# Kernel optimization log

Hardware: AMD Instinct MI355X
Metric: run time of the kernel (lower is better)

Reference implementation:

```python
import jax, jax.numpy as jnp
import numpy as np

FIELD_DIMS = (339, 5825, 64)
RANK = 128
NUM_CHANNELS = 256
BATCH = 131072
NUM_MODES = len(FIELD_DIMS)


def setup_inputs() -> dict:
    key = jax.random.key(0)
    ks = jax.random.split(key, 12)
    # per-mode in-range indices, shape (B, num_modes)
    cols = [jax.random.randint(ks[i], (BATCH,), 0, FIELD_DIMS[i]) for i in range(NUM_MODES)]
    indices = jnp.stack(cols, axis=1).astype(jnp.int64)
    # embedding tables (one per tensor mode)
    emb0 = jax.random.normal(ks[3], (FIELD_DIMS[0], RANK), jnp.float32) * 0.1
    emb1 = jax.random.normal(ks[4], (FIELD_DIMS[1], RANK), jnp.float32) * 0.1
    emb2 = jax.random.normal(ks[5], (FIELD_DIMS[2], RANK), jnp.float32) * 0.1
    # conv1: Conv2d(1, C, kernel=(rank,1)) -> weight (C, rank) after squeeze
    w1 = jax.random.normal(ks[6], (NUM_CHANNELS, RANK), jnp.float32) * (1.0 / np.sqrt(RANK))
    b1 = jnp.zeros((NUM_CHANNELS,), jnp.float32)
    # conv2: Conv2d(C, C, kernel=(1,num_modes)) -> weight (C_out, C_in, num_modes)
    w2 = jax.random.normal(ks[7], (NUM_CHANNELS, NUM_CHANNELS, NUM_MODES), jnp.float32) * (1.0 / np.sqrt(NUM_CHANNELS * NUM_MODES))
    b2 = jnp.zeros((NUM_CHANNELS,), jnp.float32)
    # aggregation MLP
    wfc1 = jax.random.normal(ks[8], (NUM_CHANNELS, NUM_CHANNELS), jnp.float32) * (1.0 / np.sqrt(NUM_CHANNELS))
    bfc1 = jnp.zeros((NUM_CHANNELS,), jnp.float32)
    wfc2 = jax.random.normal(ks[9], (1, NUM_CHANNELS), jnp.float32) * (1.0 / np.sqrt(NUM_CHANNELS))
    bfc2 = jnp.zeros((1,), jnp.float32)
    return {"indices": indices, "emb0": emb0, "emb1": emb1, "emb2": emb2,
            "w1": w1, "b1": b1, "w2": w2, "b2": b2,
            "wfc1": wfc1, "bfc1": bfc1, "wfc2": wfc2, "bfc2": bfc2}


def reference(indices, emb0, emb1, emb2, w1, b1, w2, b2, wfc1, bfc1, wfc2, bfc2):
    # EmbeddingModule: (B, rank, num_modes)
    x = jnp.stack([emb0[indices[:, 0]], emb1[indices[:, 1]], emb2[indices[:, 2]]], axis=2)
    # conv1 over rank dim (kernel (rank,1)): (B, C, num_modes)
    h = jax.nn.relu(jnp.einsum('brm,cr->bcm', x, w1) + b1[None, :, None])
    # conv2 over mode dim (kernel (1,num_modes)): (B, C)
    h = jax.nn.relu(jnp.einsum('bcm,dcm->bd', h, w2) + b2)
    # AggregationModule MLP
    h = jax.nn.relu(h @ wfc1.T + bfc1)
    out = jax.nn.relu(h @ wfc2.T + bfc2)  # (B, 1)
    return out.squeeze(-1)  # (B,)
```

## Files before the change

kernel.cpp:

```cpp
#include <hip/hip_runtime.h>

typedef __bf16 bf16;
typedef __bf16 bf16x4 __attribute__((ext_vector_type(4)));
typedef __bf16 bf16x8 __attribute__((ext_vector_type(8)));
typedef float  f32x4  __attribute__((ext_vector_type(4)));
typedef unsigned int uint32;

#define BT 64

#define N_EF0 (22*2048)
#define N_EF1 (365*2048)
#define N_EF2 (4*2048)
#define O_EF0 0
#define O_EF1 (O_EF0+N_EF0)
#define O_EF2 (O_EF1+N_EF1)
#define O_W1F (O_EF2+N_EF2)
#define O_W2F (O_W1F+32768)
#define O_F1  (O_W2F+196608)
#define O_F2  (O_F1+65536)
#define N_TOT (O_F2+256)

#define BYTES_BF16 ((size_t)N_TOT*2)
#define OFF_FLOAT  BYTES_BF16
#define OFF_FLAG   (OFF_FLOAT + 772*4)
#define OFF_IDX    (OFF_FLAG + 16)
#define N_IDX      (131072*3)
#define OFF_Q      (OFF_IDX + (size_t)N_IDX*4)

#define QB0 0
#define QB1 (339*256)
#define QB2 (QB1 + 5825*256)

static __device__ __forceinline__ f32x4 mfma16(bf16x8 a, bf16x8 b, f32x4 c) {
    return __builtin_amdgcn_mfma_f32_16x16x32_bf16(a, b, c, 0, 0, 0);
}

static __device__ __forceinline__ unsigned frag_off(unsigned ee, unsigned kk, unsigned nks) {
    return (((ee >> 4) * nks + (kk >> 5)) * 64u + ((kk >> 3) & 3u) * 16u + (ee & 15u)) * 8u
           + (kk & 7u);
}

__global__ __launch_bounds__(256)
void convert_all(const void* __restrict__ e0, const void* __restrict__ e1,
                 const void* __restrict__ e2, const void* __restrict__ w1r,
                 const void* __restrict__ b1r, const void* __restrict__ w2r,
                 const void* __restrict__ b2r, const void* __restrict__ f1r,
                 const void* __restrict__ fc1br, const void* __restrict__ f2r,
                 const void* __restrict__ fc2br, const void* __restrict__ idxr,
                 bf16* __restrict__ wsb, float* __restrict__ wsf,
                 int* __restrict__ flagp, int* __restrict__ idx32)
{
    __shared__ int sF;
    const int tid = threadIdx.x;
    const int bid = blockIdx.x;
    if (tid == 0) sF = 0;
    __syncthreads();

    if (bid < 256) {
        if (((const uint32*)idxr)[tid * 2 + 1] != 0) atomicOr(&sF, 1);
        __syncthreads();
        const bool i64 = (sF == 0);
        #pragma unroll
        for (int it = 0; it < 6; ++it) {
            int k = bid * 1536 + it * 256 + tid;
            if (k < N_IDX) {
                long long v = i64 ? ((const long long*)idxr)[k]
                                  : (long long)((const int*)idxr)[k];
                int m = k - (k / 3) * 3;
                long long dim = (m == 0 ? 339 : (m == 1 ? 5825 : 64));
                v = v < 0 ? 0 : (v >= dim ? dim - 1 : v);
                idx32[k] = (int)v;
            }
        }
        return;
    }

    if (tid < 64) {
        uint32 e = (((const uint32*)w1r)[tid] >> 7) & 0xffu;
        if (e > 126u) atomicOr(&sF, 1);
    }
    __syncthreads();
    const bool fp32 = (sF != 0);

    if (bid < 768) {
        const unsigned n4 = 895744u / 4u;
        for (unsigned u = (bid - 256) * 256u + tid; u < n4; u += 512u * 256u) {
            unsigned e = u * 4;
            const void* src; unsigned off, dst;
            if (e < 829952u) {
                unsigned base;
                if (e < 43392u)       { src = e0;  off = e;           base = O_EF0; }
                else if (e < 788992u) { src = e1;  off = e - 43392u;  base = O_EF1; }
                else if (e < 797184u) { src = e2;  off = e - 788992u; base = O_EF2; }
                else                  { src = w1r; off = e - 797184u; base = O_W1F; }
                dst = base + frag_off(off >> 7, off & 127u, 4u);
            } else if (e < 895488u) {
                src = f1r; off = e - 829952u;
                dst = O_F1 + frag_off(off >> 8, off & 255u, 8u);
            } else {
                src = f2r; off = e - 895488u; dst = O_F2 + off;
            }
            if (fp32) {
                float4 v = *(const float4*)((const float*)src + off);
                bf16x4 o; o[0]=(bf16)v.x; o[1]=(bf16)v.y; o[2]=(bf16)v.z; o[3]=(bf16)v.w;
                *(bf16x4*)(wsb + dst) = o;
            } else {
                *(uint2*)(wsb + dst) = *(const uint2*)((const bf16*)src + off);
            }
        }
    } else if (bid < 1008) {
        for (unsigned i = (bid - 768) * 256u + tid; i < 196608u; i += 240u * 256u) {
            unsigned m = i >> 16, r = i & 65535u;
            unsigned dt = r >> 12, ks = (r >> 9) & 7u, lane = (r >> 3) & 63u, j = r & 7u;
            unsigned d = dt * 16u + (lane & 15u);
            unsigned c = ks * 32u + (lane >> 4) * 8u + j;
            unsigned off = d * 768u + c * 3u + m;
            wsb[O_W2F + i] = fp32 ? (bf16)((const float*)w2r)[off] : ((const bf16*)w2r)[off];
        }
    } else {
        if (tid == 0) *flagp = fp32 ? 1 : 0;
        #pragma unroll
        for (int it = 0; it < 4; ++it) {
            int j = it * 256 + tid;
            if (j < 769) {
                const void* src; int off;
                if (j < 256)      { src = b1r;   off = j; }
                else if (j < 512) { src = b2r;   off = j - 256; }
                else if (j < 768) { src = fc1br; off = j - 512; }
                else              { src = fc2br; off = 0; }
                wsf[j] = fp32 ? ((const float*)src)[off] : (float)((const bf16*)src)[off];
            }
        }
    }
}

__global__ __launch_bounds__(256)
void build_q(const bf16* __restrict__ wsb, const float* __restrict__ wsf,
             bf16* __restrict__ Qt)
{
    __shared__ alignas(16) bf16 sPE[4096];

    const int tid  = threadIdx.x;
    const int wave = tid >> 6;
    const int lane = tid & 63;
    const int quad = lane >> 4;
    const int l15  = lane & 15;
    const int bid  = blockIdx.x;

    int m, tile, dim, efBase, qBase;
    if (bid < 22)       { m = 0; tile = bid;       dim = 339;  efBase = O_EF0; qBase = QB0; }
    else if (bid < 387) { m = 1; tile = bid - 22;  dim = 5825; efBase = O_EF1; qBase = QB1; }
    else                { m = 2; tile = bid - 387; dim = 64;   efBase = O_EF2; qBase = QB2; }
    const int row0 = tile * 16;

    const bf16* w1f = wsb + O_W1F;
    const bf16* w2f = wsb + O_W2F + m * 65536;
    const float* fb1 = wsf;
    const float* fb2 = wsf + 256;
    const f32x4 zero4 = {0.f, 0.f, 0.f, 0.f};

    bf16x8 be[4];
    #pragma unroll
    for (int ks = 0; ks < 4; ++ks)
        be[ks] = *(const bf16x8*)(wsb + efBase + (size_t)((tile * 4 + ks) * 64 + lane) * 8);

    #pragma unroll
    for (int mtl = 0; mtl < 4; ++mtl) {
        int mt = wave * 4 + mtl;
        f32x4 acc = zero4;
        #pragma unroll
        for (int ks = 0; ks < 4; ++ks) {
            bf16x8 aw = *(const bf16x8*)(w1f + ((mt * 4 + ks) * 64 + lane) * 8);
            acc = mfma16(aw, be[ks], acc);
        }
        const float4 bv = *(const float4*)(fb1 + mt * 16 + quad * 4);
        bf16x4 hv;
        hv[0] = (bf16)fmaxf(acc[0] + bv.x, 0.f);
        hv[1] = (bf16)fmaxf(acc[1] + bv.y, 0.f);
        hv[2] = (bf16)fmaxf(acc[2] + bv.z, 0.f);
        hv[3] = (bf16)fmaxf(acc[3] + bv.w, 0.f);
        int ksq   = mt >> 1;
        int quadq = ((mt & 1) << 1) | (quad >> 1);
        int j0    = (quad & 1) * 4;
        *(bf16x4*)(&sPE[(ksq * 64 + quadq * 16 + l15) * 8 + j0]) = hv;
    }
    __syncthreads();

    f32x4 acc2[4];
    #pragma unroll
    for (int nt = 0; nt < 4; ++nt) acc2[nt] = zero4;
    #pragma unroll
    for (int ks = 0; ks < 8; ++ks) {
        bf16x8 af = *(const bf16x8*)(&sPE[(ks * 64 + lane) * 8]);
        #pragma unroll
        for (int nt = 0; nt < 4; ++nt) {
            bf16x8 bw = *(const bf16x8*)(w2f + (size_t)(((wave * 4 + nt) * 8 + ks) * 64 + lane) * 8);
            acc2[nt] = mfma16(af, bw, acc2[nt]);
        }
    }
    #pragma unroll
    for (int nt = 0; nt < 4; ++nt) {
        int d = (wave * 4 + nt) * 16 + l15;
        const float addb = (m == 0) ? fb2[d] : 0.f;
        #pragma unroll
        for (int r = 0; r < 4; ++r) {
            int rl = quad * 4 + r;
            if (row0 + rl < dim)
                Qt[qBase + (size_t)(row0 + rl) * 256 + d] = (bf16)(acc2[nt][r] + addb);
        }
    }
}

__global__ __launch_bounds__(256, 4)
void costco_main(const bf16* __restrict__ wsb, const bf16* __restrict__ Qt,
                 const float* __restrict__ wsf, const int* __restrict__ flagp,
                 const int* __restrict__ idx32, void* __restrict__ out)
{
    __shared__ alignas(16) bf16 sH2[BT * 256];
    __shared__ float sPart[4][BT];

    const bf16* wf   = wsb + O_F1;
    const bf16* wfc2 = wsb + O_F2;
    const float* fbc1 = wsf + 512;
    const float  bfc2v = wsf[768];
    const int fp32out = *flagp;

    const int tid  = threadIdx.x;
    const int wave = tid >> 6;
    const int lane = tid & 63;
    const int quad = lane >> 4;
    const int l15  = lane & 15;
    const int bbase = blockIdx.x * BT;

    {
        const int half  = lane >> 5;
        const int l31   = lane & 31;
        const int ksw   = l31 >> 2;
        const int quadw = l31 & 3;
        int i0[8], i1[8], i2[8];
        #pragma unroll
        for (int rp = 0; rp < 8; ++rp) {
            const int gb = (bbase + wave * 16 + rp * 2 + half) * 3;
            i0[rp] = idx32[gb];
            i1[rp] = idx32[gb + 1];
            i2[rp] = idx32[gb + 2];
        }
        #pragma unroll
        for (int rp = 0; rp < 8; ++rp) {
            bf16x8 a = *(const bf16x8*)(Qt + QB0 + (size_t)i0[rp] * 256 + l31 * 8);
            bf16x8 b = *(const bf16x8*)(Qt + QB1 + (size_t)i1[rp] * 256 + l31 * 8);
            bf16x8 c = *(const bf16x8*)(Qt + QB2 + (size_t)i2[rp] * 256 + l31 * 8);
            bf16x8 o;
            #pragma unroll
            for (int j = 0; j < 8; ++j)
                o[j] = (bf16)fmaxf((float)a[j] + (float)b[j] + (float)c[j], 0.f);
            const int l15r = rp * 2 + half;
            *(bf16x8*)(&sH2[((wave * 8 + ksw) * 64 + quadw * 16 + (l15r ^ ksw)) * 8]) = o;
        }
    }

    bf16x8 bfr0[4];
    #pragma unroll
    for (int nt = 0; nt < 4; ++nt)
        bfr0[nt] = *(const bf16x8*)(wf + ((size_t)((wave * 4 + nt) * 8) * 64 + lane) * 8);

    __syncthreads();

    const f32x4 zero4 = {0.f, 0.f, 0.f, 0.f};

    f32x4 acc3[4][4];
    #pragma unroll
    for (int i = 0; i < 4; ++i)
        #pragma unroll
        for (int j = 0; j < 4; ++j) acc3[i][j] = zero4;
    #pragma unroll
    for (int ks = 0; ks < 8; ++ks) {
        bf16x8 af[4], bfr[4];
        #pragma unroll
        for (int mt = 0; mt < 4; ++mt)
            af[mt] = *(const bf16x8*)(&sH2[((mt * 8 + ks) * 64 + quad * 16 + (l15 ^ ks)) * 8]);
        #pragma unroll
        for (int nt = 0; nt < 4; ++nt)
            bfr[nt] = (ks == 0) ? bfr0[nt]
                    : *(const bf16x8*)(wf + ((size_t)((wave * 4 + nt) * 8 + ks) * 64 + lane) * 8);
        #pragma unroll
        for (int mt = 0; mt < 4; ++mt)
            #pragma unroll
            for (int nt = 0; nt < 4; ++nt)
                acc3[mt][nt] = mfma16(af[mt], bfr[nt], acc3[mt][nt]);
    }

    float wv[4], bc[4];
    #pragma unroll
    for (int nt = 0; nt < 4; ++nt) {
        int e = wave * 64 + nt * 16 + l15;
        wv[nt] = (float)wfc2[e];
        bc[nt] = fbc1[e];
    }
    #pragma unroll
    for (int mt = 0; mt < 4; ++mt)
        #pragma unroll
        for (int r = 0; r < 4; ++r) {
            float p = 0.f;
            #pragma unroll
            for (int nt = 0; nt < 4; ++nt)
                p += fmaxf(acc3[mt][nt][r] + bc[nt], 0.f) * wv[nt];
            p += __shfl_xor(p, 1, 64);
            p += __shfl_xor(p, 2, 64);
            p += __shfl_xor(p, 4, 64);
            p += __shfl_xor(p, 8, 64);
            if (l15 == 0) sPart[wave][mt * 16 + quad * 4 + r] = p;
        }
    __syncthreads();

    if (tid < BT) {
        float v = sPart[0][tid] + sPart[1][tid] + sPart[2][tid] + sPart[3][tid] + bfc2v;
        v = fmaxf(v, 0.f);
        if (fp32out) ((float*)out)[bbase + tid] = v;
        else         ((bf16*)out)[bbase + tid] = (bf16)v;
    }
}

extern "C" void kernel_launch(void* const* d_in, const int* in_sizes, int n_in,
                              void* d_out, int out_size, void* d_ws, size_t ws_size,
                              hipStream_t stream) {
    char* ws = (char*)d_ws;
    bf16*  wsb   = (bf16*)ws;
    float* wsf   = (float*)(ws + OFF_FLOAT);
    int*   flagp = (int*)(ws + OFF_FLAG);
    int*   idx32 = (int*)(ws + OFF_IDX);
    bf16*  Qt    = (bf16*)(ws + OFF_Q);

    hipLaunchKernelGGL(convert_all, dim3(1009), dim3(256), 0, stream,
                       d_in[1], d_in[2], d_in[3], d_in[4], d_in[5], d_in[6],
                       d_in[7], d_in[8], d_in[9], d_in[10], d_in[11], d_in[0],
                       wsb, wsf, flagp, idx32);

    hipLaunchKernelGGL(build_q, dim3(391), dim3(256), 0, stream, wsb, wsf, Qt);

    const int B = 131072;
    hipLaunchKernelGGL(costco_main, dim3(B / BT), dim3(256), 0, stream,
                       wsb, Qt, wsf, flagp, idx32, d_out);
}
```

Measured before the change: 117.6 us.

## Read raw embeddings and w1 directly in build_q; transpose weights via LDS

```diff
diff --git a/kernel.cpp b/kernel.cpp
--- a/kernel.cpp
+++ b/kernel.cpp
@@ -8,17 +8,10 @@
 
 #define BT 64
 
-#define N_EF0 (22*2048)
-#define N_EF1 (365*2048)
-#define N_EF2 (4*2048)
-#define O_EF0 0
-#define O_EF1 (O_EF0+N_EF0)
-#define O_EF2 (O_EF1+N_EF1)
-#define O_W1F (O_EF2+N_EF2)
-#define O_W2F (O_W1F+32768)
-#define O_F1  (O_W2F+196608)
-#define O_F2  (O_F1+65536)
-#define N_TOT (O_F2+256)
+#define O_W2F 0
+#define O_F1  196608
+#define O_F2  262144
+#define N_TOT 262400
 
 #define BYTES_BF16 ((size_t)N_TOT*2)
 #define OFF_FLOAT  BYTES_BF16
@@ -35,21 +28,28 @@
     return __builtin_amdgcn_mfma_f32_16x16x32_bf16(a, b, c, 0, 0, 0);
 }
 
-static __device__ __forceinline__ unsigned frag_off(unsigned ee, unsigned kk, unsigned nks) {
-    return (((ee >> 4) * nks + (kk >> 5)) * 64u + ((kk >> 3) & 3u) * 16u + (ee & 15u)) * 8u
-           + (kk & 7u);
+static __device__ __forceinline__ bf16x8 load8(const void* p, size_t off, bool fp32) {
+    if (fp32) {
+        const float4* q = (const float4*)((const float*)p + off);
+        float4 a = q[0], b = q[1];
+        bf16x8 o;
+        o[0]=(bf16)a.x; o[1]=(bf16)a.y; o[2]=(bf16)a.z; o[3]=(bf16)a.w;
+        o[4]=(bf16)b.x; o[5]=(bf16)b.y; o[6]=(bf16)b.z; o[7]=(bf16)b.w;
+        return o;
+    }
+    return *(const bf16x8*)((const bf16*)p + off);
 }
 
 __global__ __launch_bounds__(256)
-void convert_all(const void* __restrict__ e0, const void* __restrict__ e1,
-                 const void* __restrict__ e2, const void* __restrict__ w1r,
-                 const void* __restrict__ b1r, const void* __restrict__ w2r,
-                 const void* __restrict__ b2r, const void* __restrict__ f1r,
-                 const void* __restrict__ fc1br, const void* __restrict__ f2r,
-                 const void* __restrict__ fc2br, const void* __restrict__ idxr,
+void convert_all(const void* __restrict__ w1r, const void* __restrict__ w2r,
+                 const void* __restrict__ b1r, const void* __restrict__ b2r,
+                 const void* __restrict__ f1r, const void* __restrict__ fc1br,
+                 const void* __restrict__ f2r, const void* __restrict__ fc2br,
+                 const void* __restrict__ idxr,
                  bf16* __restrict__ wsb, float* __restrict__ wsf,
                  int* __restrict__ flagp, int* __restrict__ idx32)
 {
+    __shared__ alignas(16) bf16 sT[12288];
     __shared__ int sF;
     const int tid = threadIdx.x;
     const int bid = blockIdx.x;
@@ -82,42 +82,7 @@
     __syncthreads();
     const bool fp32 = (sF != 0);
 
-    if (bid < 768) {
-        const unsigned n4 = 895744u / 4u;
-        for (unsigned u = (bid - 256) * 256u + tid; u < n4; u += 512u * 256u) {
-            unsigned e = u * 4;
-            const void* src; unsigned off, dst;
-            if (e < 829952u) {
-                unsigned base;
-                if (e < 43392u)       { src = e0;  off = e;           base = O_EF0; }
-                else if (e < 788992u) { src = e1;  off = e - 43392u;  base = O_EF1; }
-                else if (e < 797184u) { src = e2;  off = e - 788992u; base = O_EF2; }
-                else                  { src = w1r; off = e - 797184u; base = O_W1F; }
-                dst = base + frag_off(off >> 7, off & 127u, 4u);
-            } else if (e < 895488u) {
-                src = f1r; off = e - 829952u;
-                dst = O_F1 + frag_off(off >> 8, off & 255u, 8u);
-            } else {
-                src = f2r; off = e - 895488u; dst = O_F2 + off;
-            }
-            if (fp32) {
-                float4 v = *(const float4*)((const float*)src + off);
-                bf16x4 o; o[0]=(bf16)v.x; o[1]=(bf16)v.y; o[2]=(bf16)v.z; o[3]=(bf16)v.w;
-                *(bf16x4*)(wsb + dst) = o;
-            } else {
-                *(uint2*)(wsb + dst) = *(const uint2*)((const bf16*)src + off);
-            }
-        }
-    } else if (bid < 1008) {
-        for (unsigned i = (bid - 768) * 256u + tid; i < 196608u; i += 240u * 256u) {
-            unsigned m = i >> 16, r = i & 65535u;
-            unsigned dt = r >> 12, ks = (r >> 9) & 7u, lane = (r >> 3) & 63u, j = r & 7u;
-            unsigned d = dt * 16u + (lane & 15u);
-            unsigned c = ks * 32u + (lane >> 4) * 8u + j;
-            unsigned off = d * 768u + c * 3u + m;
-            wsb[O_W2F + i] = fp32 ? (bf16)((const float*)w2r)[off] : ((const bf16*)w2r)[off];
-        }
-    } else {
+    if (bid == 256) {
         if (tid == 0) *flagp = fp32 ? 1 : 0;
         #pragma unroll
         for (int it = 0; it < 4; ++it) {
@@ -131,14 +96,79 @@
                 wsf[j] = fp32 ? ((const float*)src)[off] : (float)((const bf16*)src)[off];
             }
         }
+        wsb[O_F2 + tid] = fp32 ? (bf16)((const float*)f2r)[tid]
+                               : ((const bf16*)f2r)[tid];
+    } else if (bid < 273) {
+        const int et = bid - 257;
+        #pragma unroll
+        for (int it = 0; it < 4; ++it) {
+            unsigned g = it * 1024u + tid * 4u;
+            unsigned goff = et * 4096u + g;
+            bf16 v4[4];
+            if (fp32) {
+                float4 t = *(const float4*)((const float*)f1r + goff);
+                v4[0]=(bf16)t.x; v4[1]=(bf16)t.y; v4[2]=(bf16)t.z; v4[3]=(bf16)t.w;
+            } else {
+                bf16x4 t = *(const bf16x4*)((const bf16*)f1r + goff);
+                v4[0]=t[0]; v4[1]=t[1]; v4[2]=t[2]; v4[3]=t[3];
+            }
+            #pragma unroll
+            for (int q2 = 0; q2 < 4; ++q2) {
+                unsigned e = goff + q2;
+                unsigned ee = e >> 8, kk = e & 255u;
+                unsigned slot = ((kk >> 5) * 64u + ((kk >> 3) & 3u) * 16u + (ee & 15u)) * 8u
+                                + (kk & 7u);
+                sT[slot] = v4[q2];
+            }
+        }
+        __syncthreads();
+        #pragma unroll
+        for (int it = 0; it < 2; ++it)
+            *(uint4*)(wsb + O_F1 + et * 4096 + it * 2048 + tid * 8) =
+                *(const uint4*)(&sT[it * 2048 + tid * 8]);
+    } else {
+        const int dt = bid - 273;
+        #pragma unroll
+        for (int it = 0; it < 12; ++it) {
+            unsigned g = it * 1024u + tid * 4u;
+            unsigned goff = dt * 12288u + g;
+            bf16 v4[4];
+            if (fp32) {
+                float4 t = *(const float4*)((const float*)w2r + goff);
+                v4[0]=(bf16)t.x; v4[1]=(bf16)t.y; v4[2]=(bf16)t.z; v4[3]=(bf16)t.w;
+            } else {
+                bf16x4 t = *(const bf16x4*)((const bf16*)w2r + goff);
+                v4[0]=t[0]; v4[1]=t[1]; v4[2]=t[2]; v4[3]=t[3];
+            }
+            unsigned dloc = g / 768u, rem = g - dloc * 768u;
+            #pragma unroll
+            for (int q2 = 0; q2 < 4; ++q2) {
+                unsigned rr = rem + q2;
+                unsigned c = rr / 3u, mm = rr - c * 3u;
+                unsigned slot = mm * 4096u
+                              + ((c >> 5) * 64u + ((c >> 3) & 3u) * 16u + dloc) * 8u
+                              + (c & 7u);
+                sT[slot] = v4[q2];
+            }
+        }
+        __syncthreads();
+        #pragma unroll
+        for (int it = 0; it < 6; ++it) {
+            unsigned mm = it >> 1, h = it & 1;
+            *(uint4*)(wsb + O_W2F + mm * 65536 + dt * 4096 + h * 2048 + tid * 8) =
+                *(const uint4*)(&sT[mm * 4096 + h * 2048 + tid * 8]);
+        }
     }
 }
 
 __global__ __launch_bounds__(256)
-void build_q(const bf16* __restrict__ wsb, const float* __restrict__ wsf,
-             bf16* __restrict__ Qt)
+void build_q(const void* __restrict__ e0, const void* __restrict__ e1,
+             const void* __restrict__ e2, const void* __restrict__ w1r,
+             const void* __restrict__ b1r, const void* __restrict__ b2r,
+             const bf16* __restrict__ wsb, bf16* __restrict__ Qt)
 {
     __shared__ alignas(16) bf16 sPE[4096];
+    __shared__ int sF;
 
     const int tid  = threadIdx.x;
     const int wave = tid >> 6;
@@ -147,22 +177,30 @@
     const int l15  = lane & 15;
     const int bid  = blockIdx.x;
 
-    int m, tile, dim, efBase, qBase;
-    if (bid < 22)       { m = 0; tile = bid;       dim = 339;  efBase = O_EF0; qBase = QB0; }
-    else if (bid < 387) { m = 1; tile = bid - 22;  dim = 5825; efBase = O_EF1; qBase = QB1; }
-    else                { m = 2; tile = bid - 387; dim = 64;   efBase = O_EF2; qBase = QB2; }
+    if (tid == 0) sF = 0;
+    __syncthreads();
+    if (tid < 64) {
+        uint32 e = (((const uint32*)w1r)[tid] >> 7) & 0xffu;
+        if (e > 126u) atomicOr(&sF, 1);
+    }
+    __syncthreads();
+    const bool fp32 = (sF != 0);
+
+    int m, tile, dim, qBase;
+    const void* eraw;
+    if (bid < 22)       { m = 0; tile = bid;       dim = 339;  eraw = e0; qBase = QB0; }
+    else if (bid < 387) { m = 1; tile = bid - 22;  dim = 5825; eraw = e1; qBase = QB1; }
+    else                { m = 2; tile = bid - 387; dim = 64;   eraw = e2; qBase = QB2; }
     const int row0 = tile * 16;
 
-    const bf16* w1f = wsb + O_W1F;
     const bf16* w2f = wsb + O_W2F + m * 65536;
-    const float* fb1 = wsf;
-    const float* fb2 = wsf + 256;
     const f32x4 zero4 = {0.f, 0.f, 0.f, 0.f};
 
+    int r = row0 + l15; r = r >= dim ? dim - 1 : r;
     bf16x8 be[4];
     #pragma unroll
     for (int ks = 0; ks < 4; ++ks)
-        be[ks] = *(const bf16x8*)(wsb + efBase + (size_t)((tile * 4 + ks) * 64 + lane) * 8);
+        be[ks] = load8(eraw, (size_t)r * 128 + ks * 32 + quad * 8, fp32);
 
     #pragma unroll
     for (int mtl = 0; mtl < 4; ++mtl) {
@@ -170,15 +208,22 @@
         f32x4 acc = zero4;
         #pragma unroll
         for (int ks = 0; ks < 4; ++ks) {
-            bf16x8 aw = *(const bf16x8*)(w1f + ((mt * 4 + ks) * 64 + lane) * 8);
+            bf16x8 aw = load8(w1r, (size_t)(mt * 16 + l15) * 128 + ks * 32 + quad * 8, fp32);
             acc = mfma16(aw, be[ks], acc);
         }
-        const float4 bv = *(const float4*)(fb1 + mt * 16 + quad * 4);
+        float bv[4];
+        if (fp32) {
+            float4 t = *(const float4*)((const float*)b1r + mt * 16 + quad * 4);
+            bv[0]=t.x; bv[1]=t.y; bv[2]=t.z; bv[3]=t.w;
+        } else {
+            bf16x4 t = *(const bf16x4*)((const bf16*)b1r + mt * 16 + quad * 4);
+            bv[0]=(float)t[0]; bv[1]=(float)t[1]; bv[2]=(float)t[2]; bv[3]=(float)t[3];
+        }
         bf16x4 hv;
-        hv[0] = (bf16)fmaxf(acc[0] + bv.x, 0.f);
-        hv[1] = (bf16)fmaxf(acc[1] + bv.y, 0.f);
-        hv[2] = (bf16)fmaxf(acc[2] + bv.z, 0.f);
-        hv[3] = (bf16)fmaxf(acc[3] + bv.w, 0.f);
+        hv[0] = (bf16)fmaxf(acc[0] + bv[0], 0.f);
+        hv[1] = (bf16)fmaxf(acc[1] + bv[1], 0.f);
+        hv[2] = (bf16)fmaxf(acc[2] + bv[2], 0.f);
+        hv[3] = (bf16)fmaxf(acc[3] + bv[3], 0.f);
         int ksq   = mt >> 1;
         int quadq = ((mt & 1) << 1) | (quad >> 1);
         int j0    = (quad & 1) * 4;
@@ -201,12 +246,14 @@
     #pragma unroll
     for (int nt = 0; nt < 4; ++nt) {
         int d = (wave * 4 + nt) * 16 + l15;
-        const float addb = (m == 0) ? fb2[d] : 0.f;
-        #pragma unroll
-        for (int r = 0; r < 4; ++r) {
-            int rl = quad * 4 + r;
+        float addb = 0.f;
+        if (m == 0)
+            addb = fp32 ? ((const float*)b2r)[d] : (float)((const bf16*)b2r)[d];
+        #pragma unroll
+        for (int rr = 0; rr < 4; ++rr) {
+            int rl = quad * 4 + rr;
             if (row0 + rl < dim)
-                Qt[qBase + (size_t)(row0 + rl) * 256 + d] = (bf16)(acc2[nt][r] + addb);
+                Qt[qBase + (size_t)(row0 + rl) * 256 + d] = (bf16)(acc2[nt][rr] + addb);
         }
     }
 }
@@ -331,12 +378,15 @@
     int*   idx32 = (int*)(ws + OFF_IDX);
     bf16*  Qt    = (bf16*)(ws + OFF_Q);
 
-    hipLaunchKernelGGL(convert_all, dim3(1009), dim3(256), 0, stream,
-                       d_in[1], d_in[2], d_in[3], d_in[4], d_in[5], d_in[6],
-                       d_in[7], d_in[8], d_in[9], d_in[10], d_in[11], d_in[0],
+    hipLaunchKernelGGL(convert_all, dim3(289), dim3(256), 0, stream,
+                       d_in[4] , d_in[6] , d_in[5] ,
+                       d_in[7] , d_in[8] , d_in[9] ,
+                       d_in[10] , d_in[11] , d_in[0] ,
                        wsb, wsf, flagp, idx32);
 
-    hipLaunchKernelGGL(build_q, dim3(391), dim3(256), 0, stream, wsb, wsf, Qt);
+    hipLaunchKernelGGL(build_q, dim3(391), dim3(256), 0, stream,
+                       d_in[1], d_in[2], d_in[3], d_in[4], d_in[5], d_in[7],
+                       wsb, Qt);
 
     const int B = 131072;
     hipLaunchKernelGGL(costco_main, dim3(B / BT), dim3(256), 0, stream,
```

New measurement: 128.9 us. +9.6%, slower.
